# Optimization experiments

Hardware: AMD Instinct MI355X
Metric: run time of the kernel (lower is better)

The kernel has to match this reference:

```python
import jax, jax.numpy as jnp
import numpy as np

D_MODEL = 512
NUM_HEADS = 8
HEAD_DIM = D_MODEL // NUM_HEADS
SEQ_LEN = 4096


def setup_inputs() -> dict:
    key = jax.random.key(0)
    ks = jax.random.split(key, 6)
    s = 1.0 / np.sqrt(D_MODEL)
    return {
        "x": jax.random.normal(ks[0], (SEQ_LEN, D_MODEL), jnp.float32),
        "wq": jax.random.normal(ks[1], (D_MODEL, D_MODEL), jnp.float32) * s,
        "bq": jnp.zeros((D_MODEL,), jnp.float32),
        "wk": jax.random.normal(ks[2], (D_MODEL, D_MODEL), jnp.float32) * s,
        "bk": jnp.zeros((D_MODEL,), jnp.float32),
        "wv": jax.random.normal(ks[3], (D_MODEL, D_MODEL), jnp.float32) * s,
        "bv": jnp.zeros((D_MODEL,), jnp.float32),
        "wo": jax.random.normal(ks[4], (D_MODEL, D_MODEL), jnp.float32) * s,
        "bo": jnp.zeros((D_MODEL,), jnp.float32),
    }


def reference(x, wq, bq, wk, bk, wv, bv, wo, bo):
    seq_len, d_model = x.shape
    # projections (nn.Linear: x @ W^T + b)
    q = x @ wq.T + bq
    k = x @ wk.T + bk
    v = x @ wv.T + bv
    # [seq, H, hd] -> [H, seq, hd]
    q = q.reshape(seq_len, NUM_HEADS, HEAD_DIM).transpose(1, 0, 2)
    k = k.reshape(seq_len, NUM_HEADS, HEAD_DIM).transpose(1, 0, 2)
    v = v.reshape(seq_len, NUM_HEADS, HEAD_DIM).transpose(1, 0, 2)
    scale = 1.0 / np.sqrt(HEAD_DIM).astype(np.float32)
    scores = jnp.einsum('hqd,hkd->hqk', q, k) * scale  # [H, S, S]
    causal = jnp.tril(jnp.ones((seq_len, seq_len), bool))  # True = keep
    scores = jnp.where(causal[None, :, :], scores, jnp.float32(-jnp.inf))
    attn = jax.nn.softmax(scores, axis=-1)
    out = jnp.einsum('hqk,hkd->hqd', attn, v)  # [H, S, hd]
    out = out.transpose(1, 0, 2).reshape(seq_len, d_model)
    return out @ wo.T + bo
```

## Files before the change

### kernel.cpp

```cpp
#include <hip/hip_runtime.h>

#define S_LEN 4096
#define DMODEL 512
#define NHEADS 8
#define HDIM 64

typedef unsigned short u16;
typedef __bf16 bf16x8 __attribute__((ext_vector_type(8)));
typedef float f32x4 __attribute__((ext_vector_type(4)));
typedef unsigned short ushort8v __attribute__((ext_vector_type(8)));

__device__ __forceinline__ u16 f2b(float f) {
  union { float f; unsigned u; } v;
  v.f = f;
  return (u16)((v.u + 0x7FFFu + ((v.u >> 16) & 1u)) >> 16);
}

__global__ __launch_bounds__(256)
void to_bf16_all(const float* __restrict__ x,  const float* __restrict__ wq,
                 const float* __restrict__ wk, const float* __restrict__ wv,
                 const float* __restrict__ wo,
                 u16* __restrict__ x16,  u16* __restrict__ wq16,
                 u16* __restrict__ wk16, u16* __restrict__ wv16,
                 u16* __restrict__ wo16) {
  const float* s; u16* d; int n;
  switch (blockIdx.z) {
    case 0:  s = x;  d = x16;  n = S_LEN * DMODEL;  break;
    case 1:  s = wq; d = wq16; n = DMODEL * DMODEL; break;
    case 2:  s = wk; d = wk16; n = DMODEL * DMODEL; break;
    case 3:  s = wv; d = wv16; n = DMODEL * DMODEL; break;
    default: s = wo; d = wo16; n = DMODEL * DMODEL; break;
  }
  int i = (int)(blockIdx.x * 256 + threadIdx.x) * 4;
  if (i >= n) return;
  const float4 v = *(const float4*)(s + i);
  ushort4 o;
  o.x = f2b(v.x); o.y = f2b(v.y); o.z = f2b(v.z); o.w = f2b(v.w);
  *(ushort4*)(d + i) = o;
}

template <int OUTMODE>
__device__ __forceinline__ void gemm128_body(
    const u16* __restrict__ A16, const u16* __restrict__ W16,
    const float* __restrict__ bias, void* __restrict__ Cout,
    int bm, int bn) {
  __shared__ u16 As[128][40];
  __shared__ u16 Ws[128][40];

  const int tid  = threadIdx.x;
  const int wid  = tid >> 6;
  const int lane = tid & 63;
  const int lg   = lane >> 4;
  const int lr   = lane & 15;
  const int wr   = wid >> 1;
  const int wc   = wid & 1;

  f32x4 acc[4][4] = {};

  for (int k0 = 0; k0 < DMODEL; k0 += 32) {
    __syncthreads();
    #pragma unroll
    for (int i = 0; i < 2; ++i) {
      const int idx = tid + i * 256;
      const int r   = idx >> 2;
      const int c8  = idx & 3;
      *(ushort8v*)&As[r][c8 * 8] =
          *(const ushort8v*)(A16 + (size_t)(bm + r) * DMODEL + k0 + c8 * 8);
      *(ushort8v*)&Ws[r][c8 * 8] =
          *(const ushort8v*)(W16 + (size_t)(bn + r) * DMODEL + k0 + c8 * 8);
    }
    __syncthreads();

    bf16x8 af[4], bf[4];
    #pragma unroll
    for (int mi = 0; mi < 4; ++mi)
      af[mi] = *(const bf16x8*)&As[wr * 64 + mi * 16 + lr][lg * 8];
    #pragma unroll
    for (int ni = 0; ni < 4; ++ni)
      bf[ni] = *(const bf16x8*)&Ws[wc * 64 + ni * 16 + lr][lg * 8];

    #pragma unroll
    for (int mi = 0; mi < 4; ++mi)
      #pragma unroll
      for (int ni = 0; ni < 4; ++ni)
        acc[mi][ni] = __builtin_amdgcn_mfma_f32_16x16x32_bf16(
            af[mi], bf[ni], acc[mi][ni], 0, 0, 0);
  }

  #pragma unroll
  for (int mi = 0; mi < 4; ++mi)
    #pragma unroll
    for (int ni = 0; ni < 4; ++ni) {
      const int col = bn + wc * 64 + ni * 16 + lr;
      const float bval = bias[col];
      const int row0 = bm + wr * 64 + mi * 16 + lg * 4;
      if (OUTMODE == 2) {
        ushort4 o4;
        o4.x = f2b(acc[mi][ni][0] + bval);
        o4.y = f2b(acc[mi][ni][1] + bval);
        o4.z = f2b(acc[mi][ni][2] + bval);
        o4.w = f2b(acc[mi][ni][3] + bval);
        *(ushort4*)((u16*)Cout + (size_t)col * S_LEN + row0) = o4;
      } else {
        #pragma unroll
        for (int r = 0; r < 4; ++r) {
          const float val = acc[mi][ni][r] + bval;
          if (OUTMODE == 1)
            ((u16*)Cout)[(size_t)(row0 + r) * DMODEL + col] = f2b(val);
          else
            ((float*)Cout)[(size_t)(row0 + r) * DMODEL + col] = val;
        }
      }
    }
}

__global__ __launch_bounds__(256)
void gemm_qkv(const u16* __restrict__ x16,
              const u16* __restrict__ wq16, const u16* __restrict__ wk16,
              const u16* __restrict__ wv16,
              const float* __restrict__ bq, const float* __restrict__ bk,
              const float* __restrict__ bvv,
              u16* __restrict__ Qm, u16* __restrict__ Km, u16* __restrict__ Vt) {
  const int bm = blockIdx.y * 128, bn = blockIdx.x * 128;
  if (blockIdx.z == 0)
    gemm128_body<1>(x16, wq16, bq, Qm, bm, bn);
  else if (blockIdx.z == 1)
    gemm128_body<1>(x16, wk16, bk, Km, bm, bn);
  else
    gemm128_body<2>(x16, wv16, bvv, Vt, bm, bn);
}

__global__ __launch_bounds__(256)
void gemm_o(const u16* __restrict__ Am, const u16* __restrict__ wo16,
            const float* __restrict__ bo, float* __restrict__ out) {
  gemm128_body<0>(Am, wo16, bo, out, blockIdx.y * 128, blockIdx.x * 128);
}

__global__ __launch_bounds__(256)
void flash_attn_mfma(const u16* __restrict__ Qg, const u16* __restrict__ Kg,
                     const u16* __restrict__ Vt, u16* __restrict__ Og) {
  const int id   = (int)blockIdx.x;
  const int j    = id & 255;
  const int head = j & 7;
  const int qi   = j >> 3;
  const int qb   = (id < 256) ? (63 - qi) : qi;
  const int q0   = qb * 64;
  const int tid  = threadIdx.x;
  const int wid  = tid >> 6;
  const int lane = tid & 63;
  const int lg   = lane >> 4;
  const int lr   = lane & 15;

  __shared__ u16 Ks[2][64][72];
  __shared__ u16 Vs[2][64][72];
  __shared__ u16 Ps[64][72];

  bf16x8 qa[2];
  #pragma unroll
  for (int ks = 0; ks < 2; ++ks)
    qa[ks] = *(const bf16x8*)(Qg + (size_t)(q0 + wid * 16 + lr) * DMODEL +
                              head * HDIM + ks * 32 + lg * 8);

  const int r0a = tid >> 3,           c8a = tid & 7;
  const int r0b = (tid + 256) >> 3,   c8b = tid & 7;

  ushort8v kreg[2], vreg[2];
  const u16* Kbase = Kg + head * HDIM;
  const u16* Vbase = Vt + (size_t)head * HDIM * S_LEN;

#define LOAD_TILE(k0_)                                                        \
  {                                                                           \
    kreg[0] = *(const ushort8v*)(Kbase + (size_t)((k0_) + r0a) * DMODEL + c8a * 8); \
    kreg[1] = *(const ushort8v*)(Kbase + (size_t)((k0_) + r0b) * DMODEL + c8b * 8); \
    vreg[0] = *(const ushort8v*)(Vbase + (size_t)r0a * S_LEN + (k0_) + c8a * 8);    \
    vreg[1] = *(const ushort8v*)(Vbase + (size_t)r0b * S_LEN + (k0_) + c8b * 8);    \
  }
#define STORE_TILE(buf_)                                                      \
  {                                                                           \
    *(ushort8v*)&Ks[buf_][r0a][c8a * 8] = kreg[0];                            \
    *(ushort8v*)&Ks[buf_][r0b][c8b * 8] = kreg[1];                            \
    *(ushort8v*)&Vs[buf_][r0a][c8a * 8] = vreg[0];                            \
    *(ushort8v*)&Vs[buf_][r0b][c8b * 8] = vreg[1];                            \
  }

  float l_sum[4] = {0.0f, 0.0f, 0.0f, 0.0f};
  f32x4 oacc[4] = {};
  const float SC = 0.125f * 1.44269504f;

  LOAD_TILE(0)
  STORE_TILE(0)
  __syncthreads();

  for (int kb = 0; kb <= qb; ++kb) {
    const int cur = kb & 1;
    const int k0  = kb * 64;

    if (kb < qb) LOAD_TILE(k0 + 64)

    f32x4 s[4] = {};
    __builtin_amdgcn_s_setprio(1);
    #pragma unroll
    for (int c = 0; c < 4; ++c)
      #pragma unroll
      for (int ks = 0; ks < 2; ++ks) {
        const bf16x8 kf = *(const bf16x8*)&Ks[cur][c * 16 + lr][ks * 32 + lg * 8];
        s[c] = __builtin_amdgcn_mfma_f32_16x16x32_bf16(qa[ks], kf, s[c], 0, 0, 0);
      }
    __builtin_amdgcn_s_setprio(0);

    const bool diag = (kb == qb);
    #pragma unroll
    for (int r = 0; r < 4; ++r) {
      const int rowg = q0 + wid * 16 + lg * 4 + r;
      #pragma unroll
      for (int c = 0; c < 4; ++c) {
        const int colg = k0 + c * 16 + lr;
        const float p = (!diag || colg <= rowg) ? exp2f(s[c][r] * SC) : 0.0f;
        Ps[wid * 16 + lg * 4 + r][c * 16 + lr] = f2b(p);
        l_sum[r] += p;
      }
    }

    bf16x8 pa[2];
    #pragma unroll
    for (int ks = 0; ks < 2; ++ks)
      pa[ks] = *(const bf16x8*)&Ps[wid * 16 + lr][ks * 32 + lg * 8];
    __builtin_amdgcn_s_setprio(1);
    #pragma unroll
    for (int c2 = 0; c2 < 4; ++c2)
      #pragma unroll
      for (int ks = 0; ks < 2; ++ks) {
        const bf16x8 vf = *(const bf16x8*)&Vs[cur][c2 * 16 + lr][ks * 32 + lg * 8];
        oacc[c2] = __builtin_amdgcn_mfma_f32_16x16x32_bf16(pa[ks], vf, oacc[c2], 0, 0, 0);
      }
    __builtin_amdgcn_s_setprio(0);

    if (kb < qb) {
      __syncthreads();
      STORE_TILE(1 - cur)
      __syncthreads();
    }
  }

  #pragma unroll
  for (int r = 0; r < 4; ++r) {
    float l = l_sum[r];
    #pragma unroll
    for (int off = 1; off < 16; off <<= 1)
      l += __shfl_xor(l, off, 64);
    const float inv = 1.0f / l;
    const int rowg = q0 + wid * 16 + lg * 4 + r;
    #pragma unroll
    for (int c2 = 0; c2 < 4; ++c2)
      Og[(size_t)rowg * DMODEL + head * HDIM + c2 * 16 + lr] =
          f2b(oacc[c2][r] * inv);
  }
#undef LOAD_TILE
#undef STORE_TILE
}

extern "C" void kernel_launch(void* const* d_in, const int* in_sizes, int n_in,
                              void* d_out, int out_size, void* d_ws, size_t ws_size,
                              hipStream_t stream) {
  const float* x  = (const float*)d_in[0];
  const float* wq = (const float*)d_in[1];
  const float* bq = (const float*)d_in[2];
  const float* wk = (const float*)d_in[3];
  const float* bk = (const float*)d_in[4];
  const float* wv = (const float*)d_in[5];
  const float* bv = (const float*)d_in[6];
  const float* wo = (const float*)d_in[7];
  const float* bo = (const float*)d_in[8];
  float* out = (float*)d_out;

  const size_t MAT = (size_t)S_LEN * DMODEL;
  const size_t WMAT = (size_t)DMODEL * DMODEL;
  u16* x16  = (u16*)d_ws;
  u16* wq16 = x16  + MAT;
  u16* wk16 = wq16 + WMAT;
  u16* wv16 = wk16 + WMAT;
  u16* wo16 = wv16 + WMAT;
  u16* Qm   = wo16 + WMAT;
  u16* Km   = Qm + MAT;
  u16* Vt   = Km + MAT;
  u16* Am   = Vt + MAT;

  to_bf16_all<<<dim3(2048, 1, 5), 256, 0, stream>>>(
      x, wq, wk, wv, wo, x16, wq16, wk16, wv16, wo16);

  gemm_qkv<<<dim3(DMODEL / 128, S_LEN / 128, 3), 256, 0, stream>>>(
      x16, wq16, wk16, wv16, bq, bk, bv, Qm, Km, Vt);

  flash_attn_mfma<<<512, 256, 0, stream>>>(Qm, Km, Vt, Am);

  gemm_o<<<dim3(DMODEL / 128, S_LEN / 128), 256, 0, stream>>>(Am, wo16, bo, out);
}
```

Before: 183.0 us.

## Stage GEMM and attention tiles via direct global-to-LDS loads

Both the projection GEMM and the flash attention kernel now copy tiles with `global_load_lds` (16-byte direct loads into LDS) instead of loading into registers and then storing to LDS. The LDS tiles become unpadded 32-element rows, with K/V split into two 32-column halves so each wave writes contiguously. In attention, this lets the next tile be written straight into the spare buffer and drops one barrier per iteration. It also adds MFMA priority hints in the GEMM and replaces the manual bf16 rounding of P with a native cast. The aims are to cut VGPR pressure and copy instructions and to overlap loads with compute. The risk is bank conflicts from the unpadded layout and reliance on correct vmcnt waits before barriers.

```diff
diff --git a/kernel.cpp b/kernel.cpp
--- a/kernel.cpp
+++ b/kernel.cpp
@@ -8,12 +8,17 @@
 typedef unsigned short u16;
 typedef __bf16 bf16x8 __attribute__((ext_vector_type(8)));
 typedef float f32x4 __attribute__((ext_vector_type(4)));
-typedef unsigned short ushort8v __attribute__((ext_vector_type(8)));
 
 __device__ __forceinline__ u16 f2b(float f) {
   union { float f; unsigned u; } v;
   v.f = f;
   return (u16)((v.u + 0x7FFFu + ((v.u >> 16) & 1u)) >> 16);
+}
+
+typedef const unsigned int __attribute__((address_space(1)))* gas1_u32p;
+typedef unsigned int __attribute__((address_space(3)))* las3_u32p;
+__device__ __forceinline__ void gload16(const void* g, void* l) {
+  __builtin_amdgcn_global_load_lds((gas1_u32p)g, (las3_u32p)l, 16, 0, 0);
 }
 
 __global__ __launch_bounds__(256)
@@ -44,8 +49,8 @@
     const u16* __restrict__ A16, const u16* __restrict__ W16,
     const float* __restrict__ bias, void* __restrict__ Cout,
     int bm, int bn) {
-  __shared__ u16 As[128][40];
-  __shared__ u16 Ws[128][40];
+  __shared__ __align__(16) u16 As[128 * 32];
+  __shared__ __align__(16) u16 Ws[128 * 32];
 
   const int tid  = threadIdx.x;
   const int wid  = tid >> 6;
@@ -59,32 +64,31 @@
 
   for (int k0 = 0; k0 < DMODEL; k0 += 32) {
     __syncthreads();
-    #pragma unroll
-    for (int i = 0; i < 2; ++i) {
-      const int idx = tid + i * 256;
-      const int r   = idx >> 2;
-      const int c8  = idx & 3;
-      *(ushort8v*)&As[r][c8 * 8] =
-          *(const ushort8v*)(A16 + (size_t)(bm + r) * DMODEL + k0 + c8 * 8);
-      *(ushort8v*)&Ws[r][c8 * 8] =
-          *(const ushort8v*)(W16 + (size_t)(bn + r) * DMODEL + k0 + c8 * 8);
+    {
+      const int i0 = tid, i1 = tid + 256;
+      gload16(A16 + (size_t)(bm + (i0 >> 2)) * DMODEL + k0 + (i0 & 3) * 8, &As[i0 * 8]);
+      gload16(A16 + (size_t)(bm + (i1 >> 2)) * DMODEL + k0 + (i1 & 3) * 8, &As[i1 * 8]);
+      gload16(W16 + (size_t)(bn + (i0 >> 2)) * DMODEL + k0 + (i0 & 3) * 8, &Ws[i0 * 8]);
+      gload16(W16 + (size_t)(bn + (i1 >> 2)) * DMODEL + k0 + (i1 & 3) * 8, &Ws[i1 * 8]);
     }
     __syncthreads();
 
     bf16x8 af[4], bf[4];
     #pragma unroll
     for (int mi = 0; mi < 4; ++mi)
-      af[mi] = *(const bf16x8*)&As[wr * 64 + mi * 16 + lr][lg * 8];
+      af[mi] = *(const bf16x8*)&As[(wr * 64 + mi * 16 + lr) * 32 + lg * 8];
     #pragma unroll
     for (int ni = 0; ni < 4; ++ni)
-      bf[ni] = *(const bf16x8*)&Ws[wc * 64 + ni * 16 + lr][lg * 8];
-
+      bf[ni] = *(const bf16x8*)&Ws[(wc * 64 + ni * 16 + lr) * 32 + lg * 8];
+
+    __builtin_amdgcn_s_setprio(1);
     #pragma unroll
     for (int mi = 0; mi < 4; ++mi)
       #pragma unroll
       for (int ni = 0; ni < 4; ++ni)
         acc[mi][ni] = __builtin_amdgcn_mfma_f32_16x16x32_bf16(
             af[mi], bf[ni], acc[mi][ni], 0, 0, 0);
+    __builtin_amdgcn_s_setprio(0);
   }
 
   #pragma unroll
@@ -151,9 +155,9 @@
   const int lg   = lane >> 4;
   const int lr   = lane & 15;
 
-  __shared__ u16 Ks[2][64][72];
-  __shared__ u16 Vs[2][64][72];
-  __shared__ u16 Ps[64][72];
+  __shared__ __align__(16) u16    Ks[2][2][64][32];
+  __shared__ __align__(16) u16    Vs[2][2][64][32];
+  __shared__ __align__(16) __bf16 Ps[64][72];
 
   bf16x8 qa[2];
   #pragma unroll
@@ -161,41 +165,30 @@
     qa[ks] = *(const bf16x8*)(Qg + (size_t)(q0 + wid * 16 + lr) * DMODEL +
                               head * HDIM + ks * 32 + lg * 8);
 
-  const int r0a = tid >> 3,           c8a = tid & 7;
-  const int r0b = (tid + 256) >> 3,   c8b = tid & 7;
-
-  ushort8v kreg[2], vreg[2];
+  const int sr = tid >> 2;
+  const int sc = (tid & 3) * 8;
   const u16* Kbase = Kg + head * HDIM;
   const u16* Vbase = Vt + (size_t)head * HDIM * S_LEN;
 
-#define LOAD_TILE(k0_)                                                        \
-  {                                                                           \
-    kreg[0] = *(const ushort8v*)(Kbase + (size_t)((k0_) + r0a) * DMODEL + c8a * 8); \
-    kreg[1] = *(const ushort8v*)(Kbase + (size_t)((k0_) + r0b) * DMODEL + c8b * 8); \
-    vreg[0] = *(const ushort8v*)(Vbase + (size_t)r0a * S_LEN + (k0_) + c8a * 8);    \
-    vreg[1] = *(const ushort8v*)(Vbase + (size_t)r0b * S_LEN + (k0_) + c8b * 8);    \
-  }
-#define STORE_TILE(buf_)                                                      \
-  {                                                                           \
-    *(ushort8v*)&Ks[buf_][r0a][c8a * 8] = kreg[0];                            \
-    *(ushort8v*)&Ks[buf_][r0b][c8b * 8] = kreg[1];                            \
-    *(ushort8v*)&Vs[buf_][r0a][c8a * 8] = vreg[0];                            \
-    *(ushort8v*)&Vs[buf_][r0b][c8b * 8] = vreg[1];                            \
+#define STAGE(k0_, buf_) {                                                    \
+    gload16(Kbase + (size_t)((k0_) + sr) * DMODEL + sc,      &Ks[buf_][0][sr][sc]); \
+    gload16(Kbase + (size_t)((k0_) + sr) * DMODEL + 32 + sc, &Ks[buf_][1][sr][sc]); \
+    gload16(Vbase + (size_t)sr * S_LEN + (k0_) + sc,         &Vs[buf_][0][sr][sc]); \
+    gload16(Vbase + (size_t)sr * S_LEN + (k0_) + 32 + sc,    &Vs[buf_][1][sr][sc]); \
   }
 
   float l_sum[4] = {0.0f, 0.0f, 0.0f, 0.0f};
   f32x4 oacc[4] = {};
   const float SC = 0.125f * 1.44269504f;
 
-  LOAD_TILE(0)
-  STORE_TILE(0)
+  STAGE(0, 0)
   __syncthreads();
 
   for (int kb = 0; kb <= qb; ++kb) {
     const int cur = kb & 1;
     const int k0  = kb * 64;
 
-    if (kb < qb) LOAD_TILE(k0 + 64)
+    if (kb < qb) STAGE(k0 + 64, cur ^ 1)
 
     f32x4 s[4] = {};
     __builtin_amdgcn_s_setprio(1);
@@ -203,7 +196,7 @@
     for (int c = 0; c < 4; ++c)
       #pragma unroll
       for (int ks = 0; ks < 2; ++ks) {
-        const bf16x8 kf = *(const bf16x8*)&Ks[cur][c * 16 + lr][ks * 32 + lg * 8];
+        const bf16x8 kf = *(const bf16x8*)&Ks[cur][ks][c * 16 + lr][lg * 8];
         s[c] = __builtin_amdgcn_mfma_f32_16x16x32_bf16(qa[ks], kf, s[c], 0, 0, 0);
       }
     __builtin_amdgcn_s_setprio(0);
@@ -216,7 +209,7 @@
       for (int c = 0; c < 4; ++c) {
         const int colg = k0 + c * 16 + lr;
         const float p = (!diag || colg <= rowg) ? exp2f(s[c][r] * SC) : 0.0f;
-        Ps[wid * 16 + lg * 4 + r][c * 16 + lr] = f2b(p);
+        Ps[wid * 16 + lg * 4 + r][c * 16 + lr] = (__bf16)p;
         l_sum[r] += p;
       }
     }
@@ -230,16 +223,12 @@
     for (int c2 = 0; c2 < 4; ++c2)
       #pragma unroll
       for (int ks = 0; ks < 2; ++ks) {
-        const bf16x8 vf = *(const bf16x8*)&Vs[cur][c2 * 16 + lr][ks * 32 + lg * 8];
+        const bf16x8 vf = *(const bf16x8*)&Vs[cur][ks][c2 * 16 + lr][lg * 8];
         oacc[c2] = __builtin_amdgcn_mfma_f32_16x16x32_bf16(pa[ks], vf, oacc[c2], 0, 0, 0);
       }
     __builtin_amdgcn_s_setprio(0);
 
-    if (kb < qb) {
-      __syncthreads();
-      STORE_TILE(1 - cur)
-      __syncthreads();
-    }
+    if (kb < qb) __syncthreads();
   }
 
   #pragma unroll
@@ -255,8 +244,7 @@
       Og[(size_t)rowg * DMODEL + head * HDIM + c2 * 16 + lr] =
           f2b(oacc[c2][r] * inv);
   }
-#undef LOAD_TILE
-#undef STORE_TILE
+#undef STAGE
 }
 
 extern "C" void kernel_launch(void* const* d_in, const int* in_sizes, int n_in,
```

Result: no change. 185.6 us (+1.4%).
